# Kernel optimization log

Hardware: AMD Instinct MI355X
Metric: run time of the kernel (lower is better)

Reference implementation:

```python
import jax, jax.numpy as jnp
import numpy as np

B, T, C = 2, 2048, 1024
H = 16
D = C // H  # head_dim = 64


def setup_inputs() -> dict:
    key = jax.random.key(0)
    k1, k2, k3, k4, k5 = jax.random.split(key, 5)
    s = 1.0 / np.sqrt(C)
    return {
        "x": jax.random.normal(k1, (B, T, C), dtype=jnp.float32),
        "w_qkv": jax.random.normal(k2, (C, 3 * C), dtype=jnp.float32) * s,
        "b_qkv": jax.random.normal(k3, (3 * C,), dtype=jnp.float32) * 0.01,
        "w_out": jax.random.normal(k4, (C, C), dtype=jnp.float32) * s,
        "b_out": jax.random.normal(k5, (C,), dtype=jnp.float32) * 0.01,
    }


def reference(x, w_qkv, b_qkv, w_out, b_out):
    Bx, Tx, Cx = x.shape
    qkv = x @ w_qkv + b_qkv                      # [B,T,3C]
    qkv = qkv.reshape(Bx, Tx, 3, H, D)
    q, k, v = qkv[:, :, 0], qkv[:, :, 1], qkv[:, :, 2]  # [B,T,H,D]
    # [B,H,T,T] scores with scaling
    scores = jnp.einsum("bqhd,bkhd->bhqk", q, k) / np.sqrt(D).astype(np.float32)
    causal = jnp.tril(jnp.ones((Tx, Tx), dtype=bool))
    scores = jnp.where(causal[None, None], scores, -jnp.inf)
    attn = jax.nn.softmax(scores, axis=-1)
    out = jnp.einsum("bhqk,bkhd->bqhd", attn, v).reshape(Bx, Tx, Cx)
    return out @ w_out + b_out
```

## Files before the change

kernel.cpp:

```cpp
#include <hip/hip_runtime.h>
#include <stdint.h>

typedef unsigned short u16;
typedef __attribute__((ext_vector_type(8))) short bfrag;
typedef __attribute__((ext_vector_type(4))) short bfrag4;
typedef __attribute__((ext_vector_type(4))) float f32x4;

#define MFMA_BF16 __builtin_amdgcn_mfma_f32_16x16x32_bf16

static constexpr int Bc = 2;
static constexpr int Tc = 2048;
static constexpr int Cc = 1024;
static constexpr int Hc = 16;
static constexpr int Dc = 64;
static constexpr int N3 = 3 * Cc;

__device__ __forceinline__ u16 f2bf(float f) {
    union { unsigned int i; float f; } v; v.f = f;
    unsigned int u = v.i;
    u += 0x7fffu + ((u >> 16) & 1u);
    return (u16)(u >> 16);
}
__device__ __forceinline__ unsigned int fbits(float f) {
    union { unsigned int i; float f; } v; v.f = f; return v.i;
}
__device__ __forceinline__ unsigned int pack_bf2(float hi, float lo) {
    return __builtin_amdgcn_perm(fbits(hi), fbits(lo), 0x07060302u);
}

#if __has_builtin(__builtin_amdgcn_mfma_f32_16x16x16bf16_1k)
__device__ __forceinline__ f32x4 MFMA16(bfrag4 a, bfrag4 b, f32x4 c) {
    return __builtin_amdgcn_mfma_f32_16x16x16bf16_1k(a, b, c, 0, 0, 0);
}
#elif __has_builtin(__builtin_amdgcn_mfma_f32_16x16x16_bf16)
__device__ __forceinline__ f32x4 MFMA16(bfrag4 a, bfrag4 b, f32x4 c) {
    return __builtin_amdgcn_mfma_f32_16x16x16_bf16(a, b, c, 0, 0, 0);
}
#else
__device__ __forceinline__ f32x4 MFMA16(bfrag4 a, bfrag4 b, f32x4 c) {
    bfrag a8 = {a[0], a[1], a[2], a[3], 0, 0, 0, 0};
    bfrag b8 = {b[0], b[1], b[2], b[3], 0, 0, 0, 0};
    return MFMA_BF16(a8, b8, c, 0, 0, 0);
}
#endif

__device__ __forceinline__ void async_load16(const u16* g, u16* lds) {
    __builtin_amdgcn_global_load_lds(
        (const __attribute__((address_space(1))) unsigned int*)g,
        (__attribute__((address_space(3))) unsigned int*)lds, 16, 0, 0);
}

__global__ __launch_bounds__(256) void prep(
    const float* __restrict__ x, const float* __restrict__ w_qkv,
    const float* __restrict__ w_out, u16* __restrict__ xb,
    u16* __restrict__ WqkvT, u16* __restrict__ WoutT) {
    __shared__ u16 tile[32][33];
    const int blk = blockIdx.x, tid = threadIdx.x;
    if (blk < 4096) {
        const int i = (blk * 256 + tid) * 4;
        const float4 v = *(const float4*)(x + i);
        ushort4 o;
        o.x = f2bf(v.x); o.y = f2bf(v.y); o.z = f2bf(v.z); o.w = f2bf(v.w);
        *(ushort4*)(xb + i) = o;
        return;
    }
    const int tx = tid & 31, ty = tid >> 5;
    const float* in; u16* out; int rows, cols, c0, r0;
    if (blk < 4096 + 3072) {
        const int t = blk - 4096;
        in = w_qkv; out = WqkvT; rows = 1024; cols = 3072;
        c0 = (t % 96) * 32; r0 = (t / 96) * 32;
    } else {
        const int t = blk - 7168;
        in = w_out; out = WoutT; rows = 1024; cols = 1024;
        c0 = (t & 31) * 32; r0 = (t >> 5) * 32;
    }
    for (int i = 0; i < 4; i++)
        tile[ty + 8 * i][tx] = f2bf(in[(size_t)(r0 + ty + 8 * i) * cols + c0 + tx]);
    __syncthreads();
    for (int i = 0; i < 4; i++)
        out[(size_t)(c0 + ty + 8 * i) * rows + r0 + tx] = tile[tx][ty + 8 * i];
}

__global__ void transpose_v(const u16* __restrict__ P, u16* __restrict__ Vt) {
    __shared__ u16 tile[32][33];
    const int bh = blockIdx.z, b = bh >> 4, h = bh & 15;
    const int t0 = blockIdx.x * 32, d0 = blockIdx.y * 32;
    const int tx = threadIdx.x, ty = threadIdx.y;
    const u16* src = P + (size_t)b * Tc * N3 + 2 * Cc + h * Dc;
    for (int i = 0; i < 4; i++)
        tile[ty + 8 * i][tx] = src[(size_t)(t0 + ty + 8 * i) * N3 + d0 + tx];
    __syncthreads();
    u16* dst = Vt + ((size_t)bh * Dc) * Tc;
    for (int i = 0; i < 4; i++)
        dst[(size_t)(d0 + ty + 8 * i) * Tc + t0 + tx] = tile[tx][ty + 8 * i];
}

template <int MODE>
__global__ __launch_bounds__(256) void gemm_bt(
    const u16* __restrict__ A, const u16* __restrict__ BT,
    const float* __restrict__ bias, void* __restrict__ out_p,
    int M, int Nn, int K) {
    __shared__ __align__(16) u16 As[128 * 64];
    __shared__ __align__(16) u16 Bs[128 * 64];

    const int tid  = threadIdx.x;
    const int wave = tid >> 6, lane = tid & 63;
    const int quad = lane >> 4, l16 = lane & 15;
    const int wm = wave & 1, wn = wave >> 1;
    const int m0 = blockIdx.y * 128, n0 = blockIdx.x * 128;

    f32x4 acc[4][4];
    #pragma unroll
    for (int i = 0; i < 4; i++)
        #pragma unroll
        for (int j = 0; j < 4; j++)
            acc[i][j] = (f32x4){0.f, 0.f, 0.f, 0.f};

    const int row8 = lane >> 3;
    const int c8   = ((lane & 7) ^ row8) * 8;
    const int swb  = l16 & 7;

    const u16* Ar = A  + (size_t)(m0 + wave * 32 + row8) * K + c8;
    const u16* Br = BT + (size_t)(n0 + wave * 32 + row8) * K + c8;
    u16* AsW = As + (wave * 32) * 64;
    u16* BsW = Bs + (wave * 32) * 64;

    for (int k0 = 0; k0 < K; k0 += 64) {
        #pragma unroll
        for (int j = 0; j < 4; j++) {
            async_load16(Ar + (size_t)(j * 8) * K + k0, AsW + j * 8 * 64);
            async_load16(Br + (size_t)(j * 8) * K + k0, BsW + j * 8 * 64);
        }
        __syncthreads();

        #pragma unroll
        for (int half = 0; half < 2; half++) {
            const int slot = ((quad | (half << 2)) ^ swb) * 8;
            bfrag af[4], bf[4];
            #pragma unroll
            for (int mt = 0; mt < 4; mt++)
                af[mt] = *(const bfrag*)(As + (wm * 64 + mt * 16 + l16) * 64 + slot);
            #pragma unroll
            for (int nt = 0; nt < 4; nt++)
                bf[nt] = *(const bfrag*)(Bs + (wn * 64 + nt * 16 + l16) * 64 + slot);
            #pragma unroll
            for (int mt = 0; mt < 4; mt++)
                #pragma unroll
                for (int nt = 0; nt < 4; nt++)
                    acc[mt][nt] = MFMA_BF16(af[mt], bf[nt], acc[mt][nt], 0, 0, 0);
        }
        __syncthreads();
    }

    #pragma unroll
    for (int nt = 0; nt < 4; nt++) {
        const int gn = n0 + wn * 64 + nt * 16 + l16;
        const float bv = bias[gn];
        #pragma unroll
        for (int mt = 0; mt < 4; mt++) {
            #pragma unroll
            for (int r = 0; r < 4; r++) {
                const int gm = m0 + wm * 64 + mt * 16 + quad * 4 + r;
                if (MODE == 1)
                    ((u16*)out_p)[(size_t)gm * Nn + gn] = f2bf(acc[mt][nt][r] + bv);
                else
                    ((float*)out_p)[(size_t)gm * Nn + gn] = acc[mt][nt][r] + bv;
            }
        }
    }
}

__global__ __launch_bounds__(256, 4) void attn_kernel(
    const u16* __restrict__ QKVp, const u16* __restrict__ Vt,
    u16* __restrict__ Ob) {
    __shared__ __align__(16) u16 KsF[64 * 64];
    __shared__ __align__(16) u16 VsF[64 * 64];

    const int tid  = threadIdx.x;
    const int wave = tid >> 6, lane = tid & 63;
    const int quad = lane >> 4, l16 = lane & 15;

    const int bh = blockIdx.x & 31;
    const int jq = 31 - (blockIdx.x >> 5);
    const int b = bh >> 4, h = bh & 15;
    const u16* Qp = QKVp + (size_t)b * Tc * N3 + h * Dc;
    const u16* Kp = Qp + Cc;
    const u16* Vp = Vt + (size_t)bh * Dc * Tc;

    const int qw = jq * 64 + wave * 16;

    const int row8 = lane >> 3;
    const int swz  = ((lane & 7) ^ row8) * 8;
    const int pk0 = ((quad)     ^ (l16 & 7)) * 8;
    const int pk1 = ((quad + 4) ^ (l16 & 7)) * 8;

    bfrag qf0, qf1;
    {
        const u16* qp = Qp + (size_t)(qw + l16) * N3 + quad * 8;
        qf0 = *(const bfrag*)qp;
        qf1 = *(const bfrag*)(qp + 32);
    }

    float l_i = 0.f;
    f32x4 oacc[4];
    #pragma unroll
    for (int g = 0; g < 4; g++) oacc[g] = (f32x4){0.f, 0.f, 0.f, 0.f};

    for (int t = 0; t <= jq; t++) {
        const int k0 = t * 64;
        #pragma unroll
        for (int j = 0; j < 2; j++) {
            const int rr = wave * 16 + j * 8;
            const int gr = rr + row8;
            async_load16(Kp + (size_t)(k0 + gr) * N3 + swz, KsF + rr * 64);
            async_load16(Vp + (size_t)gr * Tc + k0 + swz, VsF + rr * 64);
        }
        __syncthreads();

        f32x4 s[4];
        #pragma unroll
        for (int g = 0; g < 4; g++) {
            const u16* kb = KsF + (g * 16 + l16) * 64;
            bfrag kf0 = *(const bfrag*)(kb + pk0);
            bfrag kf1 = *(const bfrag*)(kb + pk1);
            f32x4 z = (f32x4){0.f, 0.f, 0.f, 0.f};
            z = MFMA_BF16(kf0, qf0, z, 0, 0, 0);
            z = MFMA_BF16(kf1, qf1, z, 0, 0, 0);
            s[g] = z;
        }

        #pragma unroll
        for (int g = 0; g < 4; g++)
            #pragma unroll
            for (int r = 0; r < 4; r++)
                s[g][r] = __expf(s[g][r] * 0.125f);
        if (t == jq) {
            #pragma unroll
            for (int g = 0; g < 4; g++)
                #pragma unroll
                for (int r = 0; r < 4; r++)
                    if (g * 16 + quad * 4 + r > wave * 16 + l16) s[g][r] = 0.f;
        }
        #pragma unroll
        for (int g = 0; g < 4; g++)
            l_i += s[g][0] + s[g][1] + s[g][2] + s[g][3];

        #pragma unroll
        for (int g = 0; g < 4; g++) {
            union { unsigned int u[2]; bfrag4 v; } pf;
            pf.u[0] = pack_bf2(s[g][1], s[g][0]);
            pf.u[1] = pack_bf2(s[g][3], s[g][2]);
            const int vc = ((2 * g + (quad >> 1)) ^ (l16 & 7)) * 8 + (quad & 1) * 4;
            #pragma unroll
            for (int ng = 0; ng < 4; ng++) {
                const bfrag4 vf = *(const bfrag4*)(VsF + (ng * 16 + l16) * 64 + vc);
                oacc[ng] = MFMA16(vf, pf.v, oacc[ng]);
            }
        }
        __syncthreads();
    }

    float rs = l_i;
    rs += __shfl_xor(rs, 16);
    rs += __shfl_xor(rs, 32);
    const float inv = 1.f / rs;
    const int q = qw + l16;
    u16* orow = Ob + (size_t)(b * Tc + q) * Cc + h * Dc + quad * 4;
    #pragma unroll
    for (int ng = 0; ng < 4; ng++) {
        ushort4 o;
        o.x = f2bf(oacc[ng][0] * inv);
        o.y = f2bf(oacc[ng][1] * inv);
        o.z = f2bf(oacc[ng][2] * inv);
        o.w = f2bf(oacc[ng][3] * inv);
        *(ushort4*)(orow + ng * 16) = o;
    }
}

extern "C" void kernel_launch(void* const* d_in, const int* in_sizes, int n_in,
                              void* d_out, int out_size, void* d_ws, size_t ws_size,
                              hipStream_t stream) {
    const float* x     = (const float*)d_in[0];
    const float* w_qkv = (const float*)d_in[1];
    const float* b_qkv = (const float*)d_in[2];
    const float* w_out = (const float*)d_in[3];
    const float* b_out = (const float*)d_in[4];
    float* out = (float*)d_out;
    u16* ws  = (u16*)d_ws;

    u16* xb    = ws;
    u16* WqkvT = xb    + (size_t)4096 * 1024;
    u16* WoutT = WqkvT + (size_t)3072 * 1024;
    u16* QKVp  = WoutT + (size_t)1024 * 1024;
    u16* Vt    = QKVp  + (size_t)4096 * 3072;
    u16* Ao    = xb;

    prep<<<8192, 256, 0, stream>>>(x, w_qkv, w_out, xb, WqkvT, WoutT);
    gemm_bt<1><<<dim3(3072 / 128, 4096 / 128), 256, 0, stream>>>(
        xb, WqkvT, b_qkv, QKVp, 4096, 3072, 1024);
    transpose_v<<<dim3(Tc / 32, Dc / 32, Bc * Hc), dim3(32, 8), 0, stream>>>(
        QKVp, Vt);
    attn_kernel<<<1024, 256, 0, stream>>>(QKVp, Vt, Ao);
    gemm_bt<0><<<dim3(1024 / 128, 4096 / 128), 256, 0, stream>>>(
        Ao, WoutT, b_out, out, 4096, 1024, 1024);
}
```

Measured before the change: 188.1 us.

## Double-buffer LDS tiles in GEMM and attention to overlap loads with MFMA

```diff
diff --git a/kernel.cpp b/kernel.cpp
--- a/kernel.cpp
+++ b/kernel.cpp
@@ -101,8 +101,8 @@
     const u16* __restrict__ A, const u16* __restrict__ BT,
     const float* __restrict__ bias, void* __restrict__ out_p,
     int M, int Nn, int K) {
-    __shared__ __align__(16) u16 As[128 * 64];
-    __shared__ __align__(16) u16 Bs[128 * 64];
+    __shared__ __align__(16) u16 As[2][128 * 32];
+    __shared__ __align__(16) u16 Bs[2][128 * 32];
 
     const int tid  = threadIdx.x;
     const int wave = tid >> 6, lane = tid & 63;
@@ -117,41 +117,49 @@
         for (int j = 0; j < 4; j++)
             acc[i][j] = (f32x4){0.f, 0.f, 0.f, 0.f};
 
-    const int row8 = lane >> 3;
-    const int c8   = ((lane & 7) ^ row8) * 8;
-    const int swb  = l16 & 7;
-
-    const u16* Ar = A  + (size_t)(m0 + wave * 32 + row8) * K + c8;
-    const u16* Br = BT + (size_t)(n0 + wave * 32 + row8) * K + c8;
-    u16* AsW = As + (wave * 32) * 64;
-    u16* BsW = Bs + (wave * 32) * 64;
-
-    for (int k0 = 0; k0 < K; k0 += 64) {
-        #pragma unroll
-        for (int j = 0; j < 4; j++) {
-            async_load16(Ar + (size_t)(j * 8) * K + k0, AsW + j * 8 * 64);
-            async_load16(Br + (size_t)(j * 8) * K + k0, BsW + j * 8 * 64);
-        }
+    const int rloc = 2 * (lane >> 3) + ((lane >> 2) & 1);
+    const int cg   = ((lane & 3) ^ ((lane >> 3) & 3)) * 8;
+    const int rk   = (l16 >> 1) & 3;
+    const int rodd = (l16 & 1) * 32;
+
+    const int T = K >> 5;
+    #define STAGE(t, bsel)                                                      \
+        {                                                                       \
+            const int k0_ = (t) << 5;                                           \
+            _Pragma("unroll")                                                   \
+            for (int j = 0; j < 2; j++) {                                       \
+                const int R0 = wave * 32 + j * 16;                              \
+                async_load16(A  + (size_t)(m0 + R0 + rloc) * K + k0_ + cg,      \
+                             &As[bsel][R0 * 32]);                               \
+                async_load16(BT + (size_t)(n0 + R0 + rloc) * K + k0_ + cg,      \
+                             &Bs[bsel][R0 * 32]);                               \
+            }                                                                   \
+        }
+
+    STAGE(0, 0);
+    for (int t = 0; t < T; t++) {
         __syncthreads();
-
-        #pragma unroll
-        for (int half = 0; half < 2; half++) {
-            const int slot = ((quad | (half << 2)) ^ swb) * 8;
-            bfrag af[4], bf[4];
-            #pragma unroll
-            for (int mt = 0; mt < 4; mt++)
-                af[mt] = *(const bfrag*)(As + (wm * 64 + mt * 16 + l16) * 64 + slot);
+        if (t + 1 < T) STAGE(t + 1, (t + 1) & 1);
+        const u16* Ab = As[t & 1];
+        const u16* Bb = Bs[t & 1];
+        bfrag af[4], bf[4];
+        #pragma unroll
+        for (int mt = 0; mt < 4; mt++) {
+            const int r = wm * 64 + mt * 16 + l16;
+            af[mt] = *(const bfrag*)(Ab + (r >> 1) * 64 + rodd + (quad ^ rk) * 8);
+        }
+        #pragma unroll
+        for (int nt = 0; nt < 4; nt++) {
+            const int r = wn * 64 + nt * 16 + l16;
+            bf[nt] = *(const bfrag*)(Bb + (r >> 1) * 64 + rodd + (quad ^ rk) * 8);
+        }
+        #pragma unroll
+        for (int mt = 0; mt < 4; mt++)
             #pragma unroll
             for (int nt = 0; nt < 4; nt++)
-                bf[nt] = *(const bfrag*)(Bs + (wn * 64 + nt * 16 + l16) * 64 + slot);
-            #pragma unroll
-            for (int mt = 0; mt < 4; mt++)
-                #pragma unroll
-                for (int nt = 0; nt < 4; nt++)
-                    acc[mt][nt] = MFMA_BF16(af[mt], bf[nt], acc[mt][nt], 0, 0, 0);
-        }
-        __syncthreads();
-    }
+                acc[mt][nt] = MFMA_BF16(af[mt], bf[nt], acc[mt][nt], 0, 0, 0);
+    }
+    #undef STAGE
 
     #pragma unroll
     for (int nt = 0; nt < 4; nt++) {
@@ -174,8 +182,8 @@
 __global__ __launch_bounds__(256, 4) void attn_kernel(
     const u16* __restrict__ QKVp, const u16* __restrict__ Vt,
     u16* __restrict__ Ob) {
-    __shared__ __align__(16) u16 KsF[64 * 64];
-    __shared__ __align__(16) u16 VsF[64 * 64];
+    __shared__ __align__(16) u16 KsF[2][64 * 64];
+    __shared__ __align__(16) u16 VsF[2][64 * 64];
 
     const int tid  = threadIdx.x;
     const int wave = tid >> 6, lane = tid & 63;
@@ -207,21 +215,33 @@
     #pragma unroll
     for (int g = 0; g < 4; g++) oacc[g] = (f32x4){0.f, 0.f, 0.f, 0.f};
 
+    #define STAGEKV(t, bsel)                                                    \
+        {                                                                       \
+            const int k0_ = (t) * 64;                                           \
+            _Pragma("unroll")                                                   \
+            for (int j = 0; j < 2; j++) {                                       \
+                const int rr = wave * 16 + j * 8;                               \
+                const int gr = rr + row8;                                       \
+                async_load16(Kp + (size_t)(k0_ + gr) * N3 + swz,                \
+                             &KsF[bsel][rr * 64]);                              \
+                async_load16(Vp + (size_t)gr * Tc + k0_ + swz,                  \
+                             &VsF[bsel][rr * 64]);                              \
+            }                                                                   \
+        }
+
+    STAGEKV(0, 0);
     for (int t = 0; t <= jq; t++) {
+        __syncthreads();
+        if (t < jq) STAGEKV(t + 1, (t + 1) & 1);
+        const u16* Kb = KsF[t & 1];
+        const u16* Vb = VsF[t & 1];
         const int k0 = t * 64;
-        #pragma unroll
-        for (int j = 0; j < 2; j++) {
-            const int rr = wave * 16 + j * 8;
-            const int gr = rr + row8;
-            async_load16(Kp + (size_t)(k0 + gr) * N3 + swz, KsF + rr * 64);
-            async_load16(Vp + (size_t)gr * Tc + k0 + swz, VsF + rr * 64);
-        }
-        __syncthreads();
+        (void)k0;
 
         f32x4 s[4];
         #pragma unroll
         for (int g = 0; g < 4; g++) {
-            const u16* kb = KsF + (g * 16 + l16) * 64;
+            const u16* kb = Kb + (g * 16 + l16) * 64;
             bfrag kf0 = *(const bfrag*)(kb + pk0);
             bfrag kf1 = *(const bfrag*)(kb + pk1);
             f32x4 z = (f32x4){0.f, 0.f, 0.f, 0.f};
@@ -254,12 +274,12 @@
             const int vc = ((2 * g + (quad >> 1)) ^ (l16 & 7)) * 8 + (quad & 1) * 4;
             #pragma unroll
             for (int ng = 0; ng < 4; ng++) {
-                const bfrag4 vf = *(const bfrag4*)(VsF + (ng * 16 + l16) * 64 + vc);
+                const bfrag4 vf = *(const bfrag4*)(Vb + (ng * 16 + l16) * 64 + vc);
                 oacc[ng] = MFMA16(vf, pf.v, oacc[ng]);
             }
         }
-        __syncthreads();
-    }
+    }
+    #undef STAGEKV
 
     float rs = l_i;
     rs += __shfl_xor(rs, 16);
```

Result: faster. 182.6 us (-2.9%).
